# Kernel optimization log

Hardware: AMD Instinct MI355X
Metric: run time of the kernel (lower is better)

The kernel has to match this reference:

```python
import jax, jax.numpy as jnp
import numpy as np

B, L, T = 512, 1024, 128  # batch, seq_len, n_tags


def setup_inputs() -> dict:
    key = jax.random.key(0)
    k1, k2, k3 = jax.random.split(key, 3)
    return {
        "emit_scores": jax.random.normal(k1, (B, L, T), dtype=jnp.float32),
        "transitions": jax.random.normal(k2, (T, T), dtype=jnp.float32),
        "tag_weight": jax.random.uniform(k3, (T,), dtype=jnp.float32),
    }


def _viterbi_single(emit, transitions):
    # emit: [L, T] (already scaled by tag_weight); transitions: [T, T]
    def step(prev, obs):
        # scores[i, j] = prev[i] + obs[j] + transitions[i, j]
        scores = prev[:, None] + obs[None, :] + transitions  # [T, T]
        return jnp.max(scores, axis=0), jnp.argmax(scores, axis=0).astype(jnp.int32)

    prev, bps = jax.lax.scan(step, emit[0], emit[1:])  # bps: [L-1, T]
    best_score = jnp.max(prev)
    last = jnp.argmax(prev).astype(jnp.int32)

    # Backtrace: path[t] = bps[t][path[t+1]], path[L-1] = last
    def back(idx, bp):
        nidx = bp[idx]
        return nidx, nidx

    _, rev_path = jax.lax.scan(back, last, bps, reverse=True)  # [L-1]
    path = jnp.concatenate([rev_path, last[None]])  # [L]
    return path, best_score


def reference(emit_scores, transitions, tag_weight):
    # emit_scores *= tag_weight (broadcast over tag dim), matching the torch code
    emit = emit_scores * tag_weight  # [B, L, T]
    path, best_score = jax.vmap(_viterbi_single, in_axes=(0, None))(emit, transitions)
    # path: [B, L] int32 tag indices (the original maps these to tag strings);
    # best_score: [B] Viterbi max score.
    return path, best_score
```

## Files before the change

kernel.cpp:

```cpp
#include <hip/hip_runtime.h>

#define B 512
#define L 1024
#define T 128
#define NROWS (L - 1)
#define SEG 64
#define NSEG 16

typedef unsigned char u8;
typedef float f2 __attribute__((ext_vector_type(2)));

#if __has_builtin(__builtin_elementwise_max)
#define MAX2(a, b) __builtin_elementwise_max((a), (b))
#else
static __device__ __forceinline__ f2 max2_(f2 a, f2 b) {
    f2 r; r.x = fmaxf(a.x, b.x); r.y = fmaxf(a.y, b.y); return r;
}
#define MAX2(a, b) max2_((a), (b))
#endif
#define M3(a, b, c) fmaxf(fmaxf((a), (b)), (c))

static __device__ __forceinline__ f2 pkadd(f2 a, f2 b) {
    f2 d;
    asm("v_pk_add_f32 %0, %1, %2" : "=v"(d) : "v"(a), "v"(b));
    return d;
}
static __device__ __forceinline__ float mx3(float a, float b, float c) {
    float d;
    asm("v_max3_f32 %0, %1, %2, %3" : "=v"(d) : "v"(a), "v"(b), "v"(c));
    return d;
}

#define BAR()                                                  \
    do {                                                       \
        asm volatile("s_waitcnt lgkmcnt(0)" ::: "memory");     \
        __builtin_amdgcn_s_barrier();                          \
        asm volatile("" ::: "memory");                         \
    } while (0)


__global__ __launch_bounds__(512, 4) void viterbi_fwd_val(
    const float* __restrict__ emit, const float* __restrict__ trans,
    const float* __restrict__ w, float* __restrict__ out,
    float* __restrict__ prevws, int* __restrict__ lastTag)
{
    const int b   = blockIdx.x;
    const int tid = threadIdx.x;
    const int h   = tid & 3;
    const int j   = tid >> 2;
    const int hbase = h << 5;
    const bool lane0 = (h == 0);

    __shared__ __align__(16) float prevbuf[2 * T];
    __shared__ float swv[8];
    __shared__ int   swj[8];

    f2 tc2[16];
#pragma unroll
    for (int q = 0; q < 8; ++q) {
        f2 a, c;
        a.x = trans[(size_t)(hbase + 4 * q + 0) * T + j];
        a.y = trans[(size_t)(hbase + 4 * q + 1) * T + j];
        c.x = trans[(size_t)(hbase + 4 * q + 2) * T + j];
        c.y = trans[(size_t)(hbase + 4 * q + 3) * T + j];
        tc2[2 * q] = a; tc2[2 * q + 1] = c;
    }

    const float wj = w[j];
    const size_t ebase = (size_t)b * L * T;
    float* prow = prevws + (size_t)b * NROWS * T;

    const char* prd = (const char*)prevbuf + 128 * h;
    char* pwr = (char*)prevbuf + 16 * ((j >> 2) ^ (j >> 5)) + 4 * (j & 3);

    const float e0 = emit[ebase + j] * wj;
    if (lane0) *(float*)pwr = e0;
    if (h == 1) prow[j] = e0;
    float myprev = e0;
    float r_c = emit[ebase + (size_t)T + j];
    float r_1 = emit[ebase + (size_t)2 * T + j];
    float bv_prev = 0.0f;
    BAR();

#define SVX(K_) ((K_ & 1) ? sv[(K_) >> 1].y : sv[(K_) >> 1].x)
#define STEP(T_, ROFF_, WOFF_)                                                 \
    {                                                                          \
        const int t_ = (T_);                                                   \
        if (h == 1 && t_ >= 2)                                                 \
            prow[(size_t)(t_ - 1) * T + j] = bv_prev;                          \
        const int tn_ = (t_ + 2 < L) ? (t_ + 2) : (L - 1);                     \
        const float r_2 = emit[ebase + (size_t)tn_ * T + j];                   \
        const float obs_ = r_c * wj;                                           \
        f2 od_; od_.x = obs_; od_.y = obs_;                                    \
        f2 sv[16];                                                             \
        _Pragma("unroll")                                                      \
        for (int q = 0; q < 8; ++q) {                                          \
            const float4 p = *(const float4*)(prd + (ROFF_) + 16 * (q ^ h));   \
            f2 plo; plo.x = p.x; plo.y = p.y;                                  \
            f2 phi; phi.x = p.z; phi.y = p.w;                                  \
            sv[2 * q]     = pkadd(pkadd(plo, od_), tc2[2 * q]);                \
            sv[2 * q + 1] = pkadd(pkadd(phi, od_), tc2[2 * q + 1]);            \
        }                                                                      \
        const float m0 = mx3(SVX(0),  SVX(1),  SVX(2));                        \
        const float m1 = mx3(SVX(3),  SVX(4),  SVX(5));                        \
        const float m2 = mx3(SVX(6),  SVX(7),  SVX(8));                        \
        const float m3 = mx3(SVX(9),  SVX(10), SVX(11));                       \
        const float m4 = mx3(SVX(12), SVX(13), SVX(14));                       \
        const float m5 = mx3(SVX(15), SVX(16), SVX(17));                       \
        const float m6 = mx3(SVX(18), SVX(19), SVX(20));                       \
        const float m7 = mx3(SVX(21), SVX(22), SVX(23));                       \
        const float m8 = mx3(SVX(24), SVX(25), SVX(26));                       \
        const float m9 = mx3(SVX(27), SVX(28), SVX(29));                       \
        const float m10 = fmaxf(SVX(30), SVX(31));                             \
        const float n0 = mx3(m0, m1, m2);                                      \
        const float n1 = mx3(m3, m4, m5);                                      \
        const float n2 = mx3(m6, m7, m8);                                      \
        const float n3 = fmaxf(m9, m10);                                       \
        float bv = fmaxf(mx3(n0, n1, n2), n3);                                 \
        bv = fmaxf(bv, __shfl_xor(bv, 1));                                     \
        bv = fmaxf(bv, __shfl_xor(bv, 2));                                     \
        if (lane0) *(float*)(pwr + (WOFF_)) = bv;                              \
        myprev = bv;                                                           \
        bv_prev = bv;                                                          \
        r_c = r_1; r_1 = r_2;                                                  \
        BAR();                                                                 \
    }

    int t = 1;
    while (t + 1 < L) {
        STEP(t, 0, 512)
        STEP(t + 1, 512, 0)
        t += 2;
    }
    STEP(1023, 0, 512)
#undef STEP
#undef SVX

    float rv = myprev; int rj = j;
#pragma unroll
    for (int m = 4; m <= 32; m <<= 1) {
        const float pv = __shfl_xor(rv, m);
        const int   pj = __shfl_xor(rj, m);
        if (pv > rv || (pv == rv && pj < rj)) { rv = pv; rj = pj; }
    }
    if ((tid & 63) == 0) { swv[tid >> 6] = rv; swj[tid >> 6] = rj; }
    __syncthreads();
    if (tid == 0) {
        float fv = swv[0]; int fj = swj[0];
#pragma unroll
        for (int wv = 1; wv < 8; ++wv) {
            if (swv[wv] > fv || (swv[wv] == fv && swj[wv] < fj)) {
                fv = swv[wv]; fj = swj[wv];
            }
        }
        out[(size_t)B * L + b] = fv;
        out[(size_t)b * L + (L - 1)] = (float)fj;
        lastTag[b] = fj;
    }
}

__global__ __launch_bounds__(64, 1) void backtrace(
    const float* __restrict__ emit, const float* __restrict__ trans,
    const float* __restrict__ w, const float* __restrict__ prevws,
    const int* __restrict__ lastTag, float* __restrict__ out)
{
    const int b = blockIdx.x;
    const int lane = threadIdx.x;
    __shared__ float transT[T * T];

#pragma unroll 4
    for (int it = 0; it < (T * T) / 64; ++it) {
        const int k = it * 64 + lane;
        const int i = k >> 7, jj = k & 127;
        transT[jj * T + (i ^ (jj & 31))] = trans[k];
    }

    const float w0 = w[lane], w1 = w[lane + 64];
    const size_t pbase = (size_t)b * NROWS * T;
    const size_t ebase = (size_t)b * L * T;
    const size_t obase = (size_t)b * L;

    float rp0[8], rp1[8], re0[8], re1[8];
#pragma unroll
    for (int k = 0; k < 8; ++k) {
        rp0[k] = prevws[pbase + (size_t)(1022 - k) * T + lane];
        rp1[k] = prevws[pbase + (size_t)(1022 - k) * T + lane + 64];
        re0[k] = emit[ebase + (size_t)(1023 - k) * T + lane];
        re1[k] = emit[ebase + (size_t)(1023 - k) * T + lane + 64];
    }

    int idx = lastTag[b];
    const float bsc = out[(size_t)B * L + b];
    float pp0 = bsc, pp1 = bsc;
    __syncthreads();

    int r = 1022;

#define BODY(U_)                                                               \
    {                                                                          \
        const float c0_ = rp0[U_], c1_ = rp1[U_];                              \
        const float e0_ = re0[U_], e1_ = re1[U_];                              \
        const int pr = (r >= 8) ? (r - 8) : 0;                                 \
        rp0[U_] = prevws[pbase + (size_t)pr * T + lane];                       \
        rp1[U_] = prevws[pbase + (size_t)pr * T + lane + 64];                  \
        re0[U_] = emit[ebase + (size_t)(pr + 1) * T + lane];                   \
        re1[U_] = emit[ebase + (size_t)(pr + 1) * T + lane + 64];              \
        const int sl = idx & 63;                                               \
        const bool lo = idx < 64;                                              \
        const float bv  = __shfl(lo ? pp0 : pp1, sl);                          \
        const float ew0 = e0_ * w0, ew1 = e1_ * w1;                            \
        const float obs = __shfl(lo ? ew0 : ew1, sl);                          \
        const int xc = lane ^ (idx & 31);                                      \
        const float t0 = transT[idx * T + xc];                                 \
        const float t1 = transT[idx * T + 64 + xc];                            \
        const float s0 = (c0_ + obs) + t0;                                     \
        const float s1 = (c1_ + obs) + t1;                                     \
        const unsigned long long m0 = __ballot(s0 == bv);                      \
        const unsigned long long m1 = __ballot(s1 == bv);                      \
        idx = (m0 != 0ULL) ? __builtin_ctzll(m0)                               \
                           : 64 + __builtin_ctzll(m1);                         \
        if (lane == 0) out[obase + r] = (float)idx;                            \
        pp0 = c0_; pp1 = c1_;                                                  \
        --r;                                                                   \
    }

#pragma unroll 1
    for (int g = 0; g < 127; ++g) {
        BODY(0) BODY(1) BODY(2) BODY(3) BODY(4) BODY(5) BODY(6) BODY(7)
    }
    BODY(0) BODY(1) BODY(2) BODY(3) BODY(4) BODY(5) BODY(6)
#undef BODY
}

__global__ __launch_bounds__(512, 4) void viterbi_fwd_slow(
    const float* __restrict__ emit, const float* __restrict__ trans,
    const float* __restrict__ w, float* __restrict__ out,
    u8* __restrict__ bps, int* __restrict__ lastTag)
{
    const int b   = blockIdx.x;
    const int tid = threadIdx.x;
    const int h   = tid & 3;
    const int j   = tid >> 2;
    const int hbase = h << 5;
    const bool lane0 = (h == 0);
    const int INF = 0x7fffffff;

    __shared__ __align__(16) float prevbuf[2 * T];
    __shared__ float swv[8];
    __shared__ int   swj[8];

    f2 tc2[16];
#pragma unroll
    for (int q = 0; q < 8; ++q) {
        f2 a, c;
        a.x = trans[(size_t)(hbase + 4 * q + 0) * T + j];
        a.y = trans[(size_t)(hbase + 4 * q + 1) * T + j];
        c.x = trans[(size_t)(hbase + 4 * q + 2) * T + j];
        c.y = trans[(size_t)(hbase + 4 * q + 3) * T + j];
        tc2[2 * q] = a; tc2[2 * q + 1] = c;
    }

    const float wj = w[j];
    const size_t ebase = (size_t)b * L * T;
    u8* bprow = bps + (size_t)b * NROWS * T;

    const char* prd = (const char*)prevbuf + 128 * h;
    char* pwr = (char*)prevbuf + 16 * ((j >> 2) ^ (j >> 5)) + 4 * (j & 3);

    const float e0 = emit[ebase + j] * wj;
    if (lane0) *(float*)pwr = e0;
    float myprev = e0;
    float raw_cur = emit[ebase + (size_t)T + j];
    int bidx_prev = 0;
    __syncthreads();

#define STEP(T_, ROFF_, WOFF_)                                                 \
    {                                                                          \
        const int t_ = (T_);                                                   \
        if (lane0 && t_ >= 2)                                                  \
            bprow[(size_t)(t_ - 2) * T + j] = (u8)bidx_prev;                   \
        const int tn_ = (t_ + 1 < L) ? (t_ + 1) : (L - 1);                     \
        const float raw_next_ = emit[ebase + (size_t)tn_ * T + j];             \
        const float obs_ = raw_cur * wj;                                       \
        f2 od_; od_.x = obs_; od_.y = obs_;                                    \
        f2 sv[16];                                                             \
        _Pragma("unroll")                                                      \
        for (int q = 0; q < 8; ++q) {                                          \
            const float4 p = *(const float4*)(prd + (ROFF_) + 16 * (q ^ h));   \
            f2 plo; plo.x = p.x; plo.y = p.y;                                  \
            f2 phi; phi.x = p.z; phi.y = p.w;                                  \
            sv[2 * q]     = (plo + od_) + tc2[2 * q];                          \
            sv[2 * q + 1] = (phi + od_) + tc2[2 * q + 1];                      \
        }                                                                      \
        float cm[4]; int loc[4];                                               \
        _Pragma("unroll")                                                      \
        for (int c = 0; c < 4; ++c) {                                          \
            const float s0 = sv[4 * c + 0].x, s1 = sv[4 * c + 0].y;            \
            const float s2 = sv[4 * c + 1].x, s3 = sv[4 * c + 1].y;            \
            const float s4 = sv[4 * c + 2].x, s5 = sv[4 * c + 2].y;            \
            const float s6 = sv[4 * c + 3].x, s7 = sv[4 * c + 3].y;            \
            const float m = M3(M3(s0, s1, s2), M3(s3, s4, s5),                 \
                               fmaxf(s6, s7));                                 \
            int k = 0;                                                         \
            k = (s7 == m) ? 7 : k; k = (s6 == m) ? 6 : k;                      \
            k = (s5 == m) ? 5 : k; k = (s4 == m) ? 4 : k;                      \
            k = (s3 == m) ? 3 : k; k = (s2 == m) ? 2 : k;                      \
            k = (s1 == m) ? 1 : k;                                             \
            cm[c] = m; loc[c] = 8 * c + k;                                     \
        }                                                                      \
        float bv = fmaxf(fmaxf(cm[0], cm[1]), fmaxf(cm[2], cm[3]));            \
        const int l0 = (cm[0] == bv) ? loc[0] : INF;                           \
        const int l1 = (cm[1] == bv) ? loc[1] : INF;                           \
        const int l2 = (cm[2] == bv) ? loc[2] : INF;                           \
        const int l3 = (cm[3] == bv) ? loc[3] : INF;                           \
        const int lm = min(min(min(l0, l1), l2), l3);                          \
        int gi = hbase + lm;                                                   \
        const float lv = bv;                                                   \
        bv = fmaxf(bv, __shfl_xor(bv, 1));                                     \
        bv = fmaxf(bv, __shfl_xor(bv, 2));                                     \
        int ii = (lv == bv) ? gi : INF;                                        \
        ii = min(ii, __shfl_xor(ii, 1));                                       \
        ii = min(ii, __shfl_xor(ii, 2));                                       \
        if (lane0) *(float*)(pwr + (WOFF_)) = bv;                              \
        myprev = bv;                                                           \
        bidx_prev = ii;                                                        \
        raw_cur = raw_next_;                                                   \
        __syncthreads();                                                       \
    }

    int t = 1;
    while (t + 1 < L) {
        STEP(t, 0, 512)
        STEP(t + 1, 512, 0)
        t += 2;
    }
    STEP(1023, 0, 512)
#undef STEP

    if (lane0) bprow[(size_t)(NROWS - 1) * T + j] = (u8)bidx_prev;

    float rv = myprev; int rj = j;
#pragma unroll
    for (int m = 4; m <= 32; m <<= 1) {
        const float pv = __shfl_xor(rv, m);
        const int   pj = __shfl_xor(rj, m);
        if (pv > rv || (pv == rv && pj < rj)) { rv = pv; rj = pj; }
    }
    if ((tid & 63) == 0) { swv[tid >> 6] = rv; swj[tid >> 6] = rj; }
    __syncthreads();
    if (tid == 0) {
        float fv = swv[0]; int fj = swj[0];
#pragma unroll
        for (int wv = 1; wv < 8; ++wv) {
            if (swv[wv] > fv || (swv[wv] == fv && swj[wv] < fj)) {
                fv = swv[wv]; fj = swj[wv];
            }
        }
        out[(size_t)B * L + b] = fv;
        out[(size_t)b * L + (L - 1)] = (float)fj;
        lastTag[b] = fj;
    }
}

__global__ __launch_bounds__(T) void segcomp(const u8* __restrict__ bps,
                                             u8* __restrict__ comp)
{
    const int s = blockIdx.x & (NSEG - 1);
    const int b = blockIdx.x >> 4;
    const int r0 = s * SEG;
    const int cnt = (NROWS - r0 < SEG) ? (NROWS - r0) : SEG;

    __shared__ __align__(16) u8 rows[SEG * T];
    const uint4* src = (const uint4*)(bps + ((size_t)b * NROWS + r0) * T);
    uint4* dst = (uint4*)rows;
    const int nvec = cnt * (T / 16);
    for (int k = threadIdx.x; k < nvec; k += T) dst[k] = src[k];
    __syncthreads();

    int x = threadIdx.x;
    for (int k = cnt - 1; k >= 0; --k) x = rows[k * T + x];
    comp[((size_t)b * NSEG + s) * T + threadIdx.x] = (u8)x;
}

__global__ void chainseg(const u8* __restrict__ comp,
                         const int* __restrict__ lastTag,
                         float* __restrict__ out)
{
    const int b = blockIdx.x * blockDim.x + threadIdx.x;
    if (b >= B) return;
    int e = lastTag[b];
#pragma unroll 1
    for (int s = NSEG - 1; s >= 0; --s) {
        e = comp[((size_t)b * NSEG + s) * T + e];
        out[(size_t)b * L + s * SEG] = (float)e;
    }
}

__global__ __launch_bounds__(T) void fillseg(const u8* __restrict__ bps,
                                             const int* __restrict__ lastTag,
                                             float* __restrict__ out)
{
    const int s = blockIdx.x & (NSEG - 1);
    const int b = blockIdx.x >> 4;
    const int r0 = s * SEG;
    const int cnt = (NROWS - r0 < SEG) ? (NROWS - r0) : SEG;

    __shared__ __align__(16) u8 rows[SEG * T];
    const uint4* src = (const uint4*)(bps + ((size_t)b * NROWS + r0) * T);
    uint4* dst = (uint4*)rows;
    const int nvec = cnt * (T / 16);
    for (int k = threadIdx.x; k < nvec; k += T) dst[k] = src[k];
    __syncthreads();

    if (threadIdx.x == 0) {
        int e = (s == NSEG - 1) ? lastTag[b]
                                : (int)out[(size_t)b * L + (size_t)(s + 1) * SEG];
        for (int k = cnt - 1; k >= 1; --k) {
            e = rows[k * T + e];
            out[(size_t)b * L + r0 + k] = (float)e;
        }
    }
}

extern "C" void kernel_launch(void* const* d_in, const int* in_sizes, int n_in,
                              void* d_out, int out_size, void* d_ws, size_t ws_size,
                              hipStream_t stream)
{
    const float* emit  = (const float*)d_in[0];
    const float* trans = (const float*)d_in[1];
    const float* w     = (const float*)d_in[2];
    float* out = (float*)d_out;

    const size_t prev_bytes = (size_t)B * NROWS * T * sizeof(float);
    const size_t need_fast  = prev_bytes + B * sizeof(int);

    if (ws_size >= need_fast) {
        float* prevws  = (float*)d_ws;
        int*   lastTag = (int*)((char*)d_ws + prev_bytes);
        viterbi_fwd_val<<<B, 512, 0, stream>>>(emit, trans, w, out, prevws, lastTag);
        backtrace<<<B, 64, 0, stream>>>(emit, trans, w, prevws, lastTag, out);
    } else {
        u8*  bps     = (u8*)d_ws;
        u8*  comp    = bps + (size_t)B * NROWS * T;
        int* lastTag = (int*)(comp + (size_t)B * NSEG * T);
        viterbi_fwd_slow<<<B, 512, 0, stream>>>(emit, trans, w, out, bps, lastTag);
        segcomp<<<B * NSEG, T, 0, stream>>>(bps, comp);
        chainseg<<<2, 256, 0, stream>>>(comp, lastTag, out);
        fillseg<<<B * NSEG, T, 0, stream>>>(bps, lastTag, out);
    }
}
```

Before: 861.8 us.

## Split each tag's max across eight lanes and reduce with DPP/swizzle

The forward Viterbi kernel now uses 1024 threads per sequence, with 8 lanes per destination tag each covering 16 predecessor states instead of 4 lanes covering 32. This halves the serial add/max chain per step, and the per-tag lane reduction uses DPP moves plus a ds_swizzle in place of __shfl_xor. The cost is more threads per block, more LDS reads per step, and a 1024-thread barrier every step, which could limit occupancy or raise barrier cost.

```diff
diff --git a/kernel.cpp b/kernel.cpp
--- a/kernel.cpp
+++ b/kernel.cpp
@@ -10,14 +10,6 @@
 typedef unsigned char u8;
 typedef float f2 __attribute__((ext_vector_type(2)));
 
-#if __has_builtin(__builtin_elementwise_max)
-#define MAX2(a, b) __builtin_elementwise_max((a), (b))
-#else
-static __device__ __forceinline__ f2 max2_(f2 a, f2 b) {
-    f2 r; r.x = fmaxf(a.x, b.x); r.y = fmaxf(a.y, b.y); return r;
-}
-#define MAX2(a, b) max2_((a), (b))
-#endif
 #define M3(a, b, c) fmaxf(fmaxf((a), (b)), (c))
 
 static __device__ __forceinline__ f2 pkadd(f2 a, f2 b) {
@@ -30,6 +22,13 @@
     asm("v_max3_f32 %0, %1, %2, %3" : "=v"(d) : "v"(a), "v"(b), "v"(c));
     return d;
 }
+
+#define DPPMAX(v, CTRL)                                                        \
+    fmaxf((v), __int_as_float(__builtin_amdgcn_mov_dpp(                        \
+                   __float_as_int(v), (CTRL), 0xf, 0xf, true)))
+#define SWZMAX(v)                                                              \
+    fmaxf((v), __int_as_float(__builtin_amdgcn_ds_swizzle(                     \
+                   __float_as_int(v), 0x101F)))
 
 #define BAR()                                                  \
     do {                                                       \
@@ -39,25 +38,24 @@
     } while (0)
 
 
-__global__ __launch_bounds__(512, 4) void viterbi_fwd_val(
+__global__ __launch_bounds__(1024, 8) void viterbi_fwd_val(
     const float* __restrict__ emit, const float* __restrict__ trans,
     const float* __restrict__ w, float* __restrict__ out,
     float* __restrict__ prevws, int* __restrict__ lastTag)
 {
     const int b   = blockIdx.x;
     const int tid = threadIdx.x;
-    const int h   = tid & 3;
-    const int j   = tid >> 2;
-    const int hbase = h << 5;
-    const bool lane0 = (h == 0);
+    const int h   = tid & 7;
+    const int j   = tid >> 3;
+    const int hbase = h << 4;
 
     __shared__ __align__(16) float prevbuf[2 * T];
-    __shared__ float swv[8];
-    __shared__ int   swj[8];
-
-    f2 tc2[16];
-#pragma unroll
-    for (int q = 0; q < 8; ++q) {
+    __shared__ float swv[16];
+    __shared__ int   swj[16];
+
+    f2 tc2[8];
+#pragma unroll
+    for (int q = 0; q < 4; ++q) {
         f2 a, c;
         a.x = trans[(size_t)(hbase + 4 * q + 0) * T + j];
         a.y = trans[(size_t)(hbase + 4 * q + 1) * T + j];
@@ -70,11 +68,15 @@
     const size_t ebase = (size_t)b * L * T;
     float* prow = prevws + (size_t)b * NROWS * T;
 
-    const char* prd = (const char*)prevbuf + 128 * h;
-    char* pwr = (char*)prevbuf + 16 * ((j >> 2) ^ (j >> 5)) + 4 * (j & 3);
+    const int ro0 = 16 * ((4 * h + 0) ^ ((h >> 1) & 3));
+    const int ro1 = 16 * ((4 * h + 1) ^ ((h >> 1) & 3));
+    const int ro2 = 16 * ((4 * h + 2) ^ ((h >> 1) & 3));
+    const int ro3 = 16 * ((4 * h + 3) ^ ((h >> 1) & 3));
+    const char* prdb = (const char*)prevbuf;
+    char* pwr = (char*)prevbuf + 16 * ((j >> 2) ^ ((j >> 5) & 3)) + 4 * (j & 3);
 
     const float e0 = emit[ebase + j] * wj;
-    if (lane0) *(float*)pwr = e0;
+    if (h == 0) *(float*)pwr = e0;
     if (h == 1) prow[j] = e0;
     float myprev = e0;
     float r_c = emit[ebase + (size_t)T + j];
@@ -82,44 +84,47 @@
     float bv_prev = 0.0f;
     BAR();
 
-#define SVX(K_) ((K_ & 1) ? sv[(K_) >> 1].y : sv[(K_) >> 1].x)
 #define STEP(T_, ROFF_, WOFF_)                                                 \
     {                                                                          \
         const int t_ = (T_);                                                   \
-        if (h == 1 && t_ >= 2)                                                 \
+        if (h == 1 && t_ >= 2)                        \
             prow[(size_t)(t_ - 1) * T + j] = bv_prev;                          \
         const int tn_ = (t_ + 2 < L) ? (t_ + 2) : (L - 1);                     \
         const float r_2 = emit[ebase + (size_t)tn_ * T + j];                   \
         const float obs_ = r_c * wj;                                           \
         f2 od_; od_.x = obs_; od_.y = obs_;                                    \
-        f2 sv[16];                                                             \
-        _Pragma("unroll")                                                      \
-        for (int q = 0; q < 8; ++q) {                                          \
-            const float4 p = *(const float4*)(prd + (ROFF_) + 16 * (q ^ h));   \
-            f2 plo; plo.x = p.x; plo.y = p.y;                                  \
-            f2 phi; phi.x = p.z; phi.y = p.w;                                  \
-            sv[2 * q]     = pkadd(pkadd(plo, od_), tc2[2 * q]);                \
-            sv[2 * q + 1] = pkadd(pkadd(phi, od_), tc2[2 * q + 1]);            \
-        }                                                                      \
-        const float m0 = mx3(SVX(0),  SVX(1),  SVX(2));                        \
-        const float m1 = mx3(SVX(3),  SVX(4),  SVX(5));                        \
-        const float m2 = mx3(SVX(6),  SVX(7),  SVX(8));                        \
-        const float m3 = mx3(SVX(9),  SVX(10), SVX(11));                       \
-        const float m4 = mx3(SVX(12), SVX(13), SVX(14));                       \
-        const float m5 = mx3(SVX(15), SVX(16), SVX(17));                       \
-        const float m6 = mx3(SVX(18), SVX(19), SVX(20));                       \
-        const float m7 = mx3(SVX(21), SVX(22), SVX(23));                       \
-        const float m8 = mx3(SVX(24), SVX(25), SVX(26));                       \
-        const float m9 = mx3(SVX(27), SVX(28), SVX(29));                       \
-        const float m10 = fmaxf(SVX(30), SVX(31));                             \
+        const float4 p0 = *(const float4*)(prdb + (ROFF_) + ro0);              \
+        const float4 p1 = *(const float4*)(prdb + (ROFF_) + ro1);              \
+        const float4 p2 = *(const float4*)(prdb + (ROFF_) + ro2);              \
+        const float4 p3 = *(const float4*)(prdb + (ROFF_) + ro3);              \
+        f2 q0; q0.x = p0.x; q0.y = p0.y;                                       \
+        f2 q1; q1.x = p0.z; q1.y = p0.w;                                       \
+        f2 q2; q2.x = p1.x; q2.y = p1.y;                                       \
+        f2 q3; q3.x = p1.z; q3.y = p1.w;                                       \
+        f2 q4; q4.x = p2.x; q4.y = p2.y;                                       \
+        f2 q5; q5.x = p2.z; q5.y = p2.w;                                       \
+        f2 q6; q6.x = p3.x; q6.y = p3.y;                                       \
+        f2 q7; q7.x = p3.z; q7.y = p3.w;                                       \
+        const f2 v0 = pkadd(pkadd(q0, od_), tc2[0]);                           \
+        const f2 v1 = pkadd(pkadd(q1, od_), tc2[1]);                           \
+        const f2 v2 = pkadd(pkadd(q2, od_), tc2[2]);                           \
+        const f2 v3 = pkadd(pkadd(q3, od_), tc2[3]);                           \
+        const f2 v4 = pkadd(pkadd(q4, od_), tc2[4]);                           \
+        const f2 v5 = pkadd(pkadd(q5, od_), tc2[5]);                           \
+        const f2 v6 = pkadd(pkadd(q6, od_), tc2[6]);                           \
+        const f2 v7 = pkadd(pkadd(q7, od_), tc2[7]);                           \
+        const float m0 = mx3(v0.x, v0.y, v1.x);                               \
+        const float m1 = mx3(v1.y, v2.x, v2.y);                               \
+        const float m2 = mx3(v3.x, v3.y, v4.x);                               \
+        const float m3 = mx3(v4.y, v5.x, v5.y);                               \
+        const float m4 = mx3(v6.x, v6.y, v7.x);                               \
         const float n0 = mx3(m0, m1, m2);                                      \
-        const float n1 = mx3(m3, m4, m5);                                      \
-        const float n2 = mx3(m6, m7, m8);                                      \
-        const float n3 = fmaxf(m9, m10);                                       \
-        float bv = fmaxf(mx3(n0, n1, n2), n3);                                 \
-        bv = fmaxf(bv, __shfl_xor(bv, 1));                                     \
-        bv = fmaxf(bv, __shfl_xor(bv, 2));                                     \
-        if (lane0) *(float*)(pwr + (WOFF_)) = bv;                              \
+        const float n1 = fmaxf(m3, m4);                                        \
+        float bv = mx3(n0, n1, v7.y);                                          \
+        bv = DPPMAX(bv, 0xB1);                          \
+        bv = DPPMAX(bv, 0x4E);                          \
+        bv = SWZMAX(bv);                               \
+        if (h == 0) *(float*)(pwr + (WOFF_)) = bv;                             \
         myprev = bv;                                                           \
         bv_prev = bv;                                                          \
         r_c = r_1; r_1 = r_2;                                                  \
@@ -134,11 +139,10 @@
     }
     STEP(1023, 0, 512)
 #undef STEP
-#undef SVX
 
     float rv = myprev; int rj = j;
 #pragma unroll
-    for (int m = 4; m <= 32; m <<= 1) {
+    for (int m = 8; m <= 32; m <<= 1) {
         const float pv = __shfl_xor(rv, m);
         const int   pj = __shfl_xor(rj, m);
         if (pv > rv || (pv == rv && pj < rj)) { rv = pv; rj = pj; }
@@ -148,7 +152,7 @@
     if (tid == 0) {
         float fv = swv[0]; int fj = swj[0];
 #pragma unroll
-        for (int wv = 1; wv < 8; ++wv) {
+        for (int wv = 1; wv < 16; ++wv) {
             if (swv[wv] > fv || (swv[wv] == fv && swj[wv] < fj)) {
                 fv = swv[wv]; fj = swj[wv];
             }
@@ -437,7 +441,7 @@
     if (ws_size >= need_fast) {
         float* prevws  = (float*)d_ws;
         int*   lastTag = (int*)((char*)d_ws + prev_bytes);
-        viterbi_fwd_val<<<B, 512, 0, stream>>>(emit, trans, w, out, prevws, lastTag);
+        viterbi_fwd_val<<<B, 1024, 0, stream>>>(emit, trans, w, out, prevws, lastTag);
         backtrace<<<B, 64, 0, stream>>>(emit, trans, w, prevws, lastTag, out);
     } else {
         u8*  bps     = (u8*)d_ws;
```

Result: slower. 882.6 us (+2.4%).
